# Performance work log

Measured on AMD Instinct MI355X. Metric: run time of the kernel, lower is better.

Reference implementation:

```python
import jax, jax.numpy as jnp
import numpy as np

D = 1024      # input_dim
E = 8         # num_experts
H = 4096      # expert_hidden
O = 1024      # expert_out
K = 2         # top_k
N = 8192      # tokens


def setup_inputs() -> dict:
    key = jax.random.key(0)
    ks = jax.random.split(key, 10)
    s = lambda fan_in: 1.0 / np.sqrt(fan_in)
    return {
        "x": jax.random.normal(ks[0], (N, D), dtype=jnp.float32),
        # expert params, stacked over E
        "W1": jax.random.uniform(ks[1], (E, D, H), jnp.float32, -s(D), s(D)),
        "b1": jnp.zeros((E, H), jnp.float32),
        "W2": jax.random.uniform(ks[2], (E, H, O), jnp.float32, -s(H), s(H)),
        "b2": jnp.zeros((E, O), jnp.float32),
        # gate MLP: D -> 4D -> D -> E
        "G1": jax.random.uniform(ks[3], (D, 4 * D), jnp.float32, -s(D), s(D)),
        "g1": jnp.zeros((4 * D,), jnp.float32),
        "G2": jax.random.uniform(ks[4], (4 * D, D), jnp.float32, -s(4 * D), s(4 * D)),
        "g2": jnp.zeros((D,), jnp.float32),
        "G3": jax.random.uniform(ks[5], (D, E), jnp.float32, -s(D), s(D)),
        "g3": jnp.zeros((E,), jnp.float32),
    }


def reference(x, W1, b1, W2, b2, G1, g1, G2, g2, G3, g3):
    # gate logits: 3-layer MLP with ReLUs
    h = jax.nn.relu(x @ G1 + g1)
    h = jax.nn.relu(h @ G2 + g2)
    gate_logits = h @ G3 + g3                      # [N, E]

    # top-k routing: softmax over selected logits, scattered to dense [N, E]
    topv, topi = jax.lax.top_k(gate_logits, K)     # [N, K]
    top_p = jax.nn.softmax(topv, axis=1)
    rows = jnp.arange(x.shape[0])[:, None]
    p = jnp.zeros_like(gate_logits).at[rows, topi].set(top_p)  # [N, E]

    # dense all-experts MLP (faithful to torch.stack over all experts)
    hid = jax.nn.relu(jnp.einsum('nd,edh->enh', x, W1) + b1[:, None, :])  # [E, N, H]
    out = jnp.einsum('enh,eho->eno', hid, W2) + b2[:, None, :]            # [E, N, O]

    # gate-weighted combine
    y = jnp.einsum('ne,eno->no', p, out)           # [N, O]
    return (y, p)
```

## Files before the change

### kernel.cpp

```cpp
#include <hip/hip_runtime.h>
#include <stdint.h>

#define N_ 8192
#define D_ 1024
#define E_ 8
#define H_ 4096
#define O_ 1024

using f16 = _Float16;
using f16x8 = __attribute__((ext_vector_type(8))) _Float16;
using f32x4 = __attribute__((ext_vector_type(4))) float;

__device__ __forceinline__ f32x4 mfma16(f16x8 a, f16x8 b, f32x4 c) {
  return __builtin_amdgcn_mfma_f32_16x16x32_f16(a, b, c, 0, 0, 0);
}

__device__ __forceinline__ int imin(int a, int b) { return a < b ? a : b; }

__global__ void splitx_k(const float* __restrict__ in, f16* __restrict__ oh,
                         f16* __restrict__ ol, int n) {
  int i = blockIdx.x * blockDim.x + threadIdx.x;
  if (i >= n) return;
  float v = in[i];
  f16 h = (f16)v;
  oh[i] = h;
  ol[i] = (f16)((v - (float)h) * 2048.0f);
}

template <bool SPLIT>
__global__ void tcast_k(const float* __restrict__ in, f16* __restrict__ oh,
                        f16* __restrict__ ol, int R, int C) {
  __shared__ float tile[32][33];
  const int b = blockIdx.z;
  const float* inb = in + (size_t)b * R * C;
  f16* ohb = oh + (size_t)b * R * C;
  f16* olb = SPLIT ? (ol + (size_t)b * R * C) : nullptr;
  const int c0 = blockIdx.x * 32, r0 = blockIdx.y * 32;
  const int tx = threadIdx.x, ty = threadIdx.y;
#pragma unroll
  for (int j = 0; j < 4; j++)
    tile[ty + 8 * j][tx] = inb[(size_t)(r0 + ty + 8 * j) * C + (c0 + tx)];
  __syncthreads();
#pragma unroll
  for (int j = 0; j < 4; j++) {
    float v = tile[tx][ty + 8 * j];
    f16 h = (f16)v;
    size_t oi = (size_t)(c0 + ty + 8 * j) * R + (r0 + tx);
    ohb[oi] = h;
    if constexpr (SPLIT) olb[oi] = (f16)((v - (float)h) * 2048.0f);
  }
}

template <bool SPLIT, int MODE, int OUT>
__global__ __launch_bounds__(256, 4) void gemm_k(
    const f16* __restrict__ Ah, const f16* __restrict__ Al,
    const f16* __restrict__ Bh, const f16* __restrict__ Bl, size_t Bstride,
    const float* __restrict__ bias, int biasStride,
    void* __restrict__ out0, void* __restrict__ out1,
    int M, int N, int K,
    const int* __restrict__ cnt, const int* __restrict__ offs,
    const int* __restrict__ rowid) {
  const int z = blockIdx.z;
  const int rows = (MODE == 0) ? M : cnt[z];
  const int rowBase = blockIdx.x * 128;
  if (rowBase >= rows) return;
  const int colBase = blockIdx.y * 128;
  const int tid = threadIdx.x, wave = tid >> 6, lane = tid & 63;

  constexpr int NT = SPLIT ? 4 : 2;
  __shared__ __align__(16) f16 lds[NT * 8192];

  const f16* BhZ = Bh + (size_t)z * Bstride;
  const f16* BlZ = SPLIT ? (Bl + (size_t)z * Bstride) : nullptr;

  const int tile_id = SPLIT ? wave : (wave >> 1);
  constexpr int NI = SPLIT ? 16 : 8;
  const int rowHalf = SPLIT ? 0 : (wave & 1) * 64;
  const bool isA = tile_id < (SPLIT ? 2 : 1);

  const int lrow = lane >> 3;
  const int kc_l = (lane & 7) ^ lrow;

  uint32_t rb[NI];
  const f16* src;
  if (isA) {
    src = (SPLIT && tile_id == 1) ? Al : Ah;
#pragma unroll
    for (int i = 0; i < NI; ++i) {
      const int ml = rowHalf + i * 8 + lrow;
      uint32_t gr;
      if (MODE == 0) {
        gr = (uint32_t)(rowBase + ml);
      } else {
        int l0 = imin(rowBase + ml, rows - 1);
        gr = (MODE == 1) ? (uint32_t)rowid[offs[z] + l0]
                         : (uint32_t)(offs[z] + l0);
      }
      rb[i] = gr * (uint32_t)K;
    }
  } else {
    src = (SPLIT && tile_id == 3) ? BlZ : BhZ;
#pragma unroll
    for (int i = 0; i < NI; ++i) {
      const int ml = rowHalf + i * 8 + lrow;
      rb[i] = (uint32_t)(colBase + ml) * (uint32_t)K;
    }
  }

  f32x4 acc[4][4] = {};
  f32x4 acc2[SPLIT ? 4 : 1][SPLIT ? 4 : 1] = {};

  const int wr = wave >> 1, wc = wave & 1, lm = lane & 15, q4 = lane >> 4;
  const int swA = lm & 7;
  const f16* tA = lds;
  const f16* tAl = lds + 8192;
  const f16* tB = lds + (SPLIT ? 2 : 1) * 8192;
  const f16* tBl = lds + 3 * 8192;

  f16* dstBase = lds + (size_t)tile_id * 8192 + (size_t)rowHalf * 64;

  for (int kt = 0; kt < K; kt += 64) {
    if (kt) __syncthreads();
#pragma unroll
    for (int i = 0; i < NI; ++i) {
      const f16* g = src + (size_t)rb[i] + (size_t)kt + kc_l * 8;
      __builtin_amdgcn_global_load_lds(
          (const __attribute__((address_space(1))) void*)g,
          (__attribute__((address_space(3))) void*)(dstBase + i * 512), 16, 0, 0);
    }
    __syncthreads();
#pragma unroll
    for (int s = 0; s < 2; ++s) {
      const int kc = s * 4 + q4;
      const int sw = (kc ^ swA) * 8;
      f16x8 a_h[4], b_h[4];
      f16x8 a_l[SPLIT ? 4 : 1], b_l[SPLIT ? 4 : 1];
#pragma unroll
      for (int i = 0; i < 4; i++) {
        int m = wr * 64 + i * 16 + lm;
        a_h[i] = *(const f16x8*)(tA + (size_t)m * 64 + sw);
        if constexpr (SPLIT)
          a_l[i] = *(const f16x8*)(tAl + (size_t)m * 64 + sw);
      }
#pragma unroll
      for (int j = 0; j < 4; j++) {
        int n = wc * 64 + j * 16 + lm;
        b_h[j] = *(const f16x8*)(tB + (size_t)n * 64 + sw);
        if constexpr (SPLIT)
          b_l[j] = *(const f16x8*)(tBl + (size_t)n * 64 + sw);
      }
#pragma unroll
      for (int i = 0; i < 4; i++)
#pragma unroll
        for (int j = 0; j < 4; j++) {
          acc[i][j] = mfma16(a_h[i], b_h[j], acc[i][j]);
          if constexpr (SPLIT) {
            acc2[i][j] = mfma16(a_h[i], b_l[j], acc2[i][j]);
            acc2[i][j] = mfma16(a_l[i], b_h[j], acc2[i][j]);
          }
        }
    }
  }

#pragma unroll
  for (int j = 0; j < 4; j++) {
    const int n = colBase + wc * 64 + j * 16 + lm;
    const float bb = bias[(size_t)z * biasStride + n];
#pragma unroll
    for (int i = 0; i < 4; i++) {
#pragma unroll
      for (int t = 0; t < 4; t++) {
        const int lr = rowBase + wr * 64 + i * 16 + q4 * 4 + t;
        float v = acc[i][j][t];
        if constexpr (SPLIT) v += acc2[i][j][t] * (1.0f / 2048.0f);
        v += bb;
        if constexpr (OUT == 0) {
          v = fmaxf(v, 0.0f);
          f16 h = (f16)v;
          ((f16*)out0)[(size_t)lr * N + n] = h;
          ((f16*)out1)[(size_t)lr * N + n] = (f16)((v - (float)h) * 2048.0f);
        } else if constexpr (OUT == 1) {
          v = fmaxf(v, 0.0f);
          ((float*)out0)[(size_t)lr * N + n] = v;
        } else if constexpr (OUT == 2) {
          if (lr < rows) {
            v = fmaxf(v, 0.0f);
            ((f16*)out0)[((size_t)offs[z] + lr) * N + n] = (f16)v;
          }
        } else {
          if (lr < rows) {
            ((float*)out0)[((size_t)offs[z] + lr) * N + n] = v;
          }
        }
      }
    }
  }
}

__global__ void logits_k(const float* __restrict__ h2, const float* __restrict__ G3,
                         const float* __restrict__ g3, float* __restrict__ logits) {
  const int t = blockIdx.x * 4 + (threadIdx.x >> 6);
  const int lane = threadIdx.x & 63;
  float acc[8] = {};
  const float* row = h2 + (size_t)t * 1024;
  for (int k = lane; k < 1024; k += 64) {
    float hv = row[k];
    const float* g = G3 + (size_t)k * 8;
#pragma unroll
    for (int e = 0; e < 8; e++) acc[e] += hv * g[e];
  }
#pragma unroll
  for (int e = 0; e < 8; e++) {
    float v = acc[e];
    for (int o = 32; o; o >>= 1) v += __shfl_down(v, o);
    if (lane == 0) logits[(size_t)t * 8 + e] = v + g3[e];
  }
}

__global__ void top2_k(const float* __restrict__ logits, float* __restrict__ pdense,
                       int* __restrict__ ti, float* __restrict__ tp,
                       int* __restrict__ cnt) {
  int t = blockIdx.x * blockDim.x + threadIdx.x;
  if (t >= N_) return;
  float v1 = -1e30f, v2 = -1e30f;
  int i1 = 0, i2 = 0;
#pragma unroll
  for (int e = 0; e < 8; e++) {
    float v = logits[(size_t)t * 8 + e];
    if (v > v1) { v2 = v1; i2 = i1; v1 = v; i1 = e; }
    else if (v > v2) { v2 = v; i2 = e; }
  }
  float e2 = expf(v2 - v1);
  float inv = 1.0f / (1.0f + e2);
  float p1 = inv, p2 = e2 * inv;
#pragma unroll
  for (int e = 0; e < 8; e++)
    pdense[(size_t)t * 8 + e] = (e == i1) ? p1 : ((e == i2) ? p2 : 0.0f);
  ti[2 * t] = i1; ti[2 * t + 1] = i2;
  tp[2 * t] = p1; tp[2 * t + 1] = p2;
  atomicAdd(&cnt[i1], 1);
  atomicAdd(&cnt[i2], 1);
}

__global__ void prefix_k(const int* __restrict__ cnt, int* __restrict__ offs,
                         int* __restrict__ cur) {
  if (threadIdx.x == 0 && blockIdx.x == 0) {
    int s = 0;
    for (int e = 0; e < E_; e++) { offs[e] = s; cur[e] = s; s += cnt[e]; }
    offs[E_] = s;
  }
}

__global__ void place_k(const int* __restrict__ ti, int* __restrict__ cur,
                        int* __restrict__ rowid, int* __restrict__ slotof) {
  int t = blockIdx.x * blockDim.x + threadIdx.x;
  if (t >= N_) return;
#pragma unroll
  for (int k = 0; k < 2; k++) {
    int e = ti[2 * t + k];
    int slot = atomicAdd(&cur[e], 1);
    rowid[slot] = t;
    slotof[2 * t + k] = slot;
  }
}

__global__ void combine_k(const float* __restrict__ out_slots,
                          const int* __restrict__ slotof,
                          const float* __restrict__ tp, float* __restrict__ y) {
  const int t = blockIdx.x;
  const int c = threadIdx.x * 4;
  const int s0 = slotof[2 * t], s1 = slotof[2 * t + 1];
  const float p0 = tp[2 * t], p1 = tp[2 * t + 1];
  const float4 a = *(const float4*)(out_slots + (size_t)s0 * O_ + c);
  const float4 b = *(const float4*)(out_slots + (size_t)s1 * O_ + c);
  float4 r;
  r.x = p0 * a.x + p1 * b.x;
  r.y = p0 * a.y + p1 * b.y;
  r.z = p0 * a.z + p1 * b.z;
  r.w = p0 * a.w + p1 * b.w;
  *(float4*)(y + (size_t)t * O_ + c) = r;
}

extern "C" void kernel_launch(void* const* d_in, const int* in_sizes, int n_in,
                              void* d_out, int out_size, void* d_ws, size_t ws_size,
                              hipStream_t stream) {
  const float* x  = (const float*)d_in[0];
  const float* W1 = (const float*)d_in[1];
  const float* b1 = (const float*)d_in[2];
  const float* W2 = (const float*)d_in[3];
  const float* b2 = (const float*)d_in[4];
  const float* G1 = (const float*)d_in[5];
  const float* g1 = (const float*)d_in[6];
  const float* G2 = (const float*)d_in[7];
  const float* g2 = (const float*)d_in[8];
  const float* G3 = (const float*)d_in[9];
  const float* g3 = (const float*)d_in[10];

  float* y = (float*)d_out;
  float* pdense = y + (size_t)N_ * O_;

  char* w = (char*)d_ws;
  auto alloc = [&](size_t bytes) -> char* {
    char* p = w;
    w += (bytes + 255) & ~(size_t)255;
    return p;
  };
  f16* xh  = (f16*)alloc((size_t)N_ * D_ * 2);
  f16* xl  = (f16*)alloc((size_t)N_ * D_ * 2);
  f16* G1h = (f16*)alloc((size_t)D_ * H_ * 2);
  f16* G1l = (f16*)alloc((size_t)D_ * H_ * 2);
  f16* G2h = (f16*)alloc((size_t)H_ * D_ * 2);
  f16* G2l = (f16*)alloc((size_t)H_ * D_ * 2);
  f16* W1t = (f16*)alloc((size_t)E_ * D_ * H_ * 2);
  f16* W2t = (f16*)alloc((size_t)E_ * H_ * O_ * 2);
  f16* h1h = (f16*)alloc((size_t)N_ * H_ * 2);
  f16* h1l = (f16*)alloc((size_t)N_ * H_ * 2);
  float* h2 = (float*)alloc((size_t)N_ * D_ * 4);
  float* logits = (float*)alloc((size_t)N_ * E_ * 4);
  int*   ti  = (int*)alloc((size_t)N_ * 2 * 4);
  float* tp  = (float*)alloc((size_t)N_ * 2 * 4);
  int*   cnt = (int*)alloc(64);
  int*   cur = (int*)alloc(64);
  int*   offs = (int*)alloc(64);
  int*   rowid = (int*)alloc((size_t)N_ * 2 * 4);
  int*   slotof = (int*)alloc((size_t)N_ * 2 * 4);
  f16*   hid = (f16*)alloc((size_t)N_ * 2 * H_ * 2);

  float* out_slots = (float*)h1h;

  hipMemsetAsync(cnt, 0, 64, stream);

  splitx_k<<<(N_ * D_) / 256, 256, 0, stream>>>(x, xh, xl, N_ * D_);
  tcast_k<true><<<dim3(H_ / 32, D_ / 32, 1), dim3(32, 8), 0, stream>>>(G1, G1h, G1l, D_, H_);
  tcast_k<true><<<dim3(D_ / 32, H_ / 32, 1), dim3(32, 8), 0, stream>>>(G2, G2h, G2l, H_, D_);
  tcast_k<false><<<dim3(H_ / 32, D_ / 32, E_), dim3(32, 8), 0, stream>>>(W1, W1t, nullptr, D_, H_);
  tcast_k<false><<<dim3(O_ / 32, H_ / 32, E_), dim3(32, 8), 0, stream>>>(W2, W2t, nullptr, H_, O_);

  gemm_k<true, 0, 0><<<dim3(64, 32, 1), 256, 0, stream>>>(
      xh, xl, G1h, G1l, 0, g1, 0, h1h, h1l, N_, H_, D_,
      nullptr, nullptr, nullptr);
  gemm_k<true, 0, 1><<<dim3(64, 8, 1), 256, 0, stream>>>(
      h1h, h1l, G2h, G2l, 0, g2, 0, h2, nullptr, N_, D_, H_,
      nullptr, nullptr, nullptr);
  logits_k<<<N_ / 4, 256, 0, stream>>>(h2, G3, g3, logits);

  top2_k<<<N_ / 256, 256, 0, stream>>>(logits, pdense, ti, tp, cnt);
  prefix_k<<<1, 64, 0, stream>>>(cnt, offs, cur);
  place_k<<<N_ / 256, 256, 0, stream>>>(ti, cur, rowid, slotof);

  gemm_k<false, 1, 2><<<dim3(64, 32, E_), 256, 0, stream>>>(
      xh, nullptr, W1t, nullptr, (size_t)D_ * H_, b1, H_, hid, nullptr,
      N_, H_, D_, cnt, offs, rowid);
  gemm_k<false, 2, 3><<<dim3(64, 8, E_), 256, 0, stream>>>(
      hid, nullptr, W2t, nullptr, (size_t)H_ * O_, b2, O_, out_slots, nullptr,
      N_, O_, H_, cnt, offs, rowid);

  combine_k<<<N_, 256, 0, stream>>>(out_slots, slotof, tp, y);
}
```

Measured before the change: 1.956 ms.

## Double-buffer GEMM LDS tiles, remap workgroups across XCDs, stage f16 epilogue via LDS

The GEMM kernel now double-buffers its LDS tiles, issuing the async global-to-LDS loads for the next K-slice before computing on the current one, so memory latency overlaps MFMA work. Workgroup IDs are remapped so that consecutive logical tiles land on the same XCD, which should improve L2 reuse. The f16 output epilogues (OUT 0 and 2) are first staged through LDS and then written as 16-byte vector stores instead of scattered 2-byte stores. The LDS footprint doubles and launch bounds drop to 2 blocks per CU, which lowers occupancy.

```diff
diff --git a/kernel.cpp b/kernel.cpp
--- a/kernel.cpp
+++ b/kernel.cpp
@@ -52,7 +52,7 @@
 }
 
 template <bool SPLIT, int MODE, int OUT>
-__global__ __launch_bounds__(256, 4) void gemm_k(
+__global__ __launch_bounds__(256, 2) void gemm_k(
     const f16* __restrict__ Ah, const f16* __restrict__ Al,
     const f16* __restrict__ Bh, const f16* __restrict__ Bl, size_t Bstride,
     const float* __restrict__ bias, int biasStride,
@@ -60,15 +60,23 @@
     int M, int N, int K,
     const int* __restrict__ cnt, const int* __restrict__ offs,
     const int* __restrict__ rowid) {
-  const int z = blockIdx.z;
+  const uint32_t nwg = gridDim.x * gridDim.y * gridDim.z;
+  uint32_t hwid = blockIdx.x + gridDim.x * (blockIdx.y + gridDim.y * blockIdx.z);
+  uint32_t lg = ((nwg & 7) == 0) ? ((hwid & 7) * (nwg >> 3) + (hwid >> 3)) : hwid;
+  const int bX = lg % gridDim.x;
+  const uint32_t lg2 = lg / gridDim.x;
+  const int bY = lg2 % gridDim.y;
+  const int bZ = lg2 / gridDim.y;
+
+  const int z = bZ;
   const int rows = (MODE == 0) ? M : cnt[z];
-  const int rowBase = blockIdx.x * 128;
+  const int rowBase = bX * 128;
   if (rowBase >= rows) return;
-  const int colBase = blockIdx.y * 128;
+  const int colBase = bY * 128;
   const int tid = threadIdx.x, wave = tid >> 6, lane = tid & 63;
 
   constexpr int NT = SPLIT ? 4 : 2;
-  __shared__ __align__(16) f16 lds[NT * 8192];
+  __shared__ __align__(16) f16 lds[2 * NT * 8192];
 
   const f16* BhZ = Bh + (size_t)z * Bstride;
   const f16* BlZ = SPLIT ? (Bl + (size_t)z * Bstride) : nullptr;
@@ -112,23 +120,34 @@
 
   const int wr = wave >> 1, wc = wave & 1, lm = lane & 15, q4 = lane >> 4;
   const int swA = lm & 7;
-  const f16* tA = lds;
-  const f16* tAl = lds + 8192;
-  const f16* tB = lds + (SPLIT ? 2 : 1) * 8192;
-  const f16* tBl = lds + 3 * 8192;
-
-  f16* dstBase = lds + (size_t)tile_id * 8192 + (size_t)rowHalf * 64;
-
-  for (int kt = 0; kt < K; kt += 64) {
-    if (kt) __syncthreads();
+
+  const int stageOff = tile_id * 8192 + rowHalf * 64;
+
+  auto stage = [&](int b, int kt) {
+    f16* dst = lds + b * (NT * 8192) + stageOff;
 #pragma unroll
     for (int i = 0; i < NI; ++i) {
       const f16* g = src + (size_t)rb[i] + (size_t)kt + kc_l * 8;
       __builtin_amdgcn_global_load_lds(
           (const __attribute__((address_space(1))) void*)g,
-          (__attribute__((address_space(3))) void*)(dstBase + i * 512), 16, 0, 0);
-    }
-    __syncthreads();
+          (__attribute__((address_space(3))) void*)(dst + i * 512), 16, 0, 0);
+    }
+  };
+
+  const int nkt = K >> 6;
+  int buf = 0;
+  stage(0, 0);
+  __syncthreads();
+
+  for (int t = 0; t < nkt; ++t) {
+    if (t + 1 < nkt) stage(buf ^ 1, (t + 1) << 6);
+
+    const f16* base = lds + buf * (NT * 8192);
+    const f16* tA = base;
+    const f16* tAl = base + 8192;
+    const f16* tB = base + (SPLIT ? 2 : 1) * 8192;
+    const f16* tBl = base + 3 * 8192;
+
 #pragma unroll
     for (int s = 0; s < 2; ++s) {
       const int kc = s * 4 + q4;
@@ -160,36 +179,71 @@
           }
         }
     }
-  }
-
-#pragma unroll
-  for (int j = 0; j < 4; j++) {
-    const int n = colBase + wc * 64 + j * 16 + lm;
-    const float bb = bias[(size_t)z * biasStride + n];
-#pragma unroll
-    for (int i = 0; i < 4; i++) {
-#pragma unroll
-      for (int t = 0; t < 4; t++) {
-        const int lr = rowBase + wr * 64 + i * 16 + q4 * 4 + t;
-        float v = acc[i][j][t];
-        if constexpr (SPLIT) v += acc2[i][j][t] * (1.0f / 2048.0f);
-        v += bb;
-        if constexpr (OUT == 0) {
-          v = fmaxf(v, 0.0f);
-          f16 h = (f16)v;
-          ((f16*)out0)[(size_t)lr * N + n] = h;
-          ((f16*)out1)[(size_t)lr * N + n] = (f16)((v - (float)h) * 2048.0f);
-        } else if constexpr (OUT == 1) {
-          v = fmaxf(v, 0.0f);
-          ((float*)out0)[(size_t)lr * N + n] = v;
-        } else if constexpr (OUT == 2) {
-          if (lr < rows) {
+    __syncthreads();
+    buf ^= 1;
+  }
+
+  if constexpr (OUT == 0 || OUT == 2) {
+    float* lb = (float*)lds;
+#pragma unroll
+    for (int j = 0; j < 4; j++) {
+      const int n = wc * 64 + j * 16 + lm;
+      const float bb = bias[(size_t)z * biasStride + colBase + n];
+#pragma unroll
+      for (int i = 0; i < 4; i++) {
+#pragma unroll
+        for (int t = 0; t < 4; t++) {
+          const int r = wr * 64 + i * 16 + q4 * 4 + t;
+          float v = acc[i][j][t];
+          if constexpr (SPLIT) v += acc2[i][j][t] * (1.0f / 2048.0f);
+          v = fmaxf(v + bb, 0.0f);
+          lb[r * 128 + n] = v;
+        }
+      }
+    }
+    __syncthreads();
+#pragma unroll
+    for (int it = 0; it < 8; ++it) {
+      const int r = it * 16 + (tid >> 4);
+      const int c = (tid & 15) * 8;
+      const float* p = lb + r * 128 + c;
+      f16x8 hv, lv;
+#pragma unroll
+      for (int e = 0; e < 8; e++) {
+        float v = p[e];
+        f16 h = (f16)v;
+        hv[e] = h;
+        if constexpr (OUT == 0) lv[e] = (f16)((v - (float)h) * 2048.0f);
+      }
+      if constexpr (OUT == 0) {
+        *(f16x8*)((f16*)out0 + (size_t)(rowBase + r) * N + colBase + c) = hv;
+        *(f16x8*)((f16*)out1 + (size_t)(rowBase + r) * N + colBase + c) = lv;
+      } else {
+        if (rowBase + r < rows)
+          *(f16x8*)((f16*)out0 +
+                    ((size_t)offs[z] + rowBase + r) * N + colBase + c) = hv;
+      }
+    }
+  } else {
+#pragma unroll
+    for (int j = 0; j < 4; j++) {
+      const int n = colBase + wc * 64 + j * 16 + lm;
+      const float bb = bias[(size_t)z * biasStride + n];
+#pragma unroll
+      for (int i = 0; i < 4; i++) {
+#pragma unroll
+        for (int t = 0; t < 4; t++) {
+          const int lr = rowBase + wr * 64 + i * 16 + q4 * 4 + t;
+          float v = acc[i][j][t];
+          if constexpr (SPLIT) v += acc2[i][j][t] * (1.0f / 2048.0f);
+          v += bb;
+          if constexpr (OUT == 1) {
             v = fmaxf(v, 0.0f);
-            ((f16*)out0)[((size_t)offs[z] + lr) * N + n] = (f16)v;
-          }
-        } else {
-          if (lr < rows) {
-            ((float*)out0)[((size_t)offs[z] + lr) * N + n] = v;
+            ((float*)out0)[(size_t)lr * N + n] = v;
+          } else {
+            if (lr < rows) {
+              ((float*)out0)[((size_t)offs[z] + lr) * N + n] = v;
+            }
           }
         }
       }
```

Measured after the change: 1.887 ms. 3.5% less time.
